# Optimization experiments

Hardware: AMD Instinct MI355X
Metric: run time of the kernel (lower is better)

## Reference

```python
import jax, jax.numpy as jnp
import numpy as np

D_EMBED = 1024
D_CROSS = 768
N_HEADS = 16
D_HEAD = D_EMBED // N_HEADS


def setup_inputs() -> dict:
    key = jax.random.key(0)
    ks = jax.random.split(key, 10)
    s = 0.02
    return {
        "x": jax.random.normal(ks[0], (4, 4096, D_EMBED), dtype=jnp.float32),
        "y": jax.random.normal(ks[1], (4, 1024, D_CROSS), dtype=jnp.float32),
        "Wq": jax.random.normal(ks[2], (D_EMBED, D_EMBED), dtype=jnp.float32) * s,
        "bq": jnp.zeros((D_EMBED,), dtype=jnp.float32),
        "Wk": jax.random.normal(ks[3], (D_CROSS, D_EMBED), dtype=jnp.float32) * s,
        "bk": jnp.zeros((D_EMBED,), dtype=jnp.float32),
        "Wv": jax.random.normal(ks[4], (D_CROSS, D_EMBED), dtype=jnp.float32) * s,
        "bv": jnp.zeros((D_EMBED,), dtype=jnp.float32),
        "Wo": jax.random.normal(ks[5], (D_EMBED, D_EMBED), dtype=jnp.float32) * s,
        "bo": jnp.zeros((D_EMBED,), dtype=jnp.float32),
    }


def reference(x, y, Wq, bq, Wk, bk, Wv, bv, Wo, bo):
    b, sq, _ = x.shape
    skv = y.shape[1]
    # projections
    q = x @ Wq + bq   # [b, sq, d_embed]
    k = y @ Wk + bk   # [b, skv, d_embed]
    v = y @ Wv + bv   # [b, skv, d_embed]
    # split heads: [b, h, s, d_head]
    q = q.reshape(b, sq, N_HEADS, D_HEAD).transpose(0, 2, 1, 3)
    k = k.reshape(b, skv, N_HEADS, D_HEAD).transpose(0, 2, 1, 3)
    v = v.reshape(b, skv, N_HEADS, D_HEAD).transpose(0, 2, 1, 3)
    scale = 1.0 / jnp.sqrt(jnp.float32(D_HEAD))
    scores = jnp.einsum("bhqd,bhkd->bhqk", q, k) * scale
    attn = jax.nn.softmax(scores, axis=-1)
    out = jnp.einsum("bhqk,bhkd->bhqd", attn, v)
    out = out.transpose(0, 2, 1, 3).reshape(b, sq, D_EMBED)
    return out @ Wo + bo
```

## Files before the change

kernel.cpp:

```cpp
#include <hip/hip_runtime.h>

typedef unsigned short ushort_t;
typedef __attribute__((ext_vector_type(8))) __bf16 bf16x8;
typedef __attribute__((ext_vector_type(4))) float floatx4;
typedef __attribute__((ext_vector_type(8))) unsigned short ushortx8;
typedef __attribute__((ext_vector_type(4))) unsigned short ushortx4;
typedef __attribute__((ext_vector_type(4))) short short4v;
typedef __attribute__((ext_vector_type(2))) unsigned uint2v;

__device__ __forceinline__ ushort_t f2bf(float f) {
    union { float f; unsigned u; } v; v.f = f;
    unsigned r = v.u + 0x7fffu + ((v.u >> 16) & 1u);
    return (ushort_t)(r >> 16);
}

__device__ __forceinline__ void gld_lds16(const ushort_t* g, ushort_t* l) {
    __builtin_amdgcn_global_load_lds(
        (const __attribute__((address_space(1))) unsigned*)g,
        (__attribute__((address_space(3))) unsigned*)l, 16, 0, 0);
}

__device__ __forceinline__ unsigned pk_bf16(float a, float b) {
    unsigned ua = __builtin_bit_cast(unsigned, a) + 0x8000u;
    unsigned ub = __builtin_bit_cast(unsigned, b) + 0x8000u;
    return __builtin_amdgcn_perm(ub, ua, 0x07060302u);
}

__global__ __launch_bounds__(256) void prep(
    const float* __restrict__ x, const float* __restrict__ y,
    const float* __restrict__ Wq, const float* __restrict__ Wo,
    const float* __restrict__ Wk, const float* __restrict__ Wv,
    ushort_t* __restrict__ xb, ushort_t* __restrict__ yb,
    ushort_t* __restrict__ Wqt, ushort_t* __restrict__ Wot,
    ushort_t* __restrict__ Wkvt) {
    const int bid = blockIdx.x;
    if (bid < 19456) {
        const int NX = 4194304;
        int i = bid * 256 + threadIdx.x;
        float4 v; ushortx4* dst;
        if (i < NX) { v = ((const float4*)x)[i]; dst = (ushortx4*)xb + i; }
        else        { int j = i - NX; v = ((const float4*)y)[j]; dst = (ushortx4*)yb + j; }
        ushortx4 o;
        o.x = f2bf(v.x); o.y = f2bf(v.y); o.z = f2bf(v.z); o.w = f2bf(v.w);
        *dst = o;
        return;
    }
    __shared__ ushort_t t[32][33];
    const float* W; ushort_t* Wt; int K, n0, k0;
    if (bid < 21504) {
        int tt = bid - 19456;
        W = (tt >> 10) ? Wo : Wq;
        Wt = (tt >> 10) ? Wot : Wqt;
        K = 1024;
        int r = tt & 1023;
        n0 = (r & 31) * 32; k0 = (r >> 5) * 32;
    } else {
        int tt = bid - 21504;
        int z = tt / 768, r = tt - z * 768;
        W = z ? Wv : Wk;
        Wt = Wkvt + (size_t)z * 786432;
        K = 768;
        n0 = (r & 31) * 32; k0 = (r >> 5) * 32;
    }
    const int tx = threadIdx.x & 31, ty = threadIdx.x >> 5;
#pragma unroll
    for (int i = 0; i < 4; ++i)
        t[ty + 8 * i][tx] = f2bf(W[(size_t)(k0 + ty + 8 * i) * 1024 + n0 + tx]);
    __syncthreads();
#pragma unroll
    for (int i = 0; i < 4; ++i)
        Wt[(size_t)(n0 + ty + 8 * i) * K + k0 + tx] = t[tx][ty + 8 * i];
}

__device__ __forceinline__ void gemm_core(
    const ushort_t* __restrict__ A, const ushort_t* __restrict__ Bt,
    int K, int m0, int n0, ushort_t* As, ushort_t* Bs,
    floatx4 (&acc)[4][4], int tid, int wr, int wc, int quad, int l16) {
    const ushort_t* ga0 = A + (size_t)(m0 + (tid >> 2)) * K + (tid & 3) * 8;
    const ushort_t* ga1 = A + (size_t)(m0 + 64 + (tid >> 2)) * K + (tid & 3) * 8;
    const ushort_t* gb0 = Bt + (size_t)(n0 + (tid >> 2)) * K + (tid & 3) * 8;
    const ushort_t* gb1 = Bt + (size_t)(n0 + 64 + (tid >> 2)) * K + (tid & 3) * 8;
    ushort_t* la0 = As + tid * 8;
    ushort_t* la1 = As + (tid + 256) * 8;
    ushort_t* lb0 = Bs + tid * 8;
    ushort_t* lb1 = Bs + (tid + 256) * 8;

    for (int kt = 0; kt < K; kt += 32) {
        __syncthreads();
        gld_lds16(ga0, la0); gld_lds16(ga1, la1);
        gld_lds16(gb0, lb0); gld_lds16(gb1, lb1);
        ga0 += 32; ga1 += 32; gb0 += 32; gb1 += 32;
        __syncthreads();
        bf16x8 af[4], bfr[4];
#pragma unroll
        for (int i = 0; i < 4; ++i)
            af[i] = *(const bf16x8*)(As + (wr * 64 + i * 16 + l16) * 32 + quad * 8);
#pragma unroll
        for (int j = 0; j < 4; ++j)
            bfr[j] = *(const bf16x8*)(Bs + (wc * 64 + j * 16 + l16) * 32 + quad * 8);
#pragma unroll
        for (int i = 0; i < 4; ++i)
#pragma unroll
            for (int j = 0; j < 4; ++j)
                acc[i][j] = __builtin_amdgcn_mfma_f32_16x16x32_bf16(af[i], bfr[j], acc[i][j], 0, 0, 0);
    }
}

__global__ __launch_bounds__(256) void proj(
    const ushort_t* __restrict__ xb, const ushort_t* __restrict__ yb,
    const ushort_t* __restrict__ Wqt, const ushort_t* __restrict__ Wkvt,
    const float* __restrict__ bq, const float* __restrict__ bk, const float* __restrict__ bv,
    ushort_t* __restrict__ Qc, ushort_t* __restrict__ Kc, ushort_t* __restrict__ Vc,
    float qscale) {
    __shared__ __align__(16) ushort_t As[128 * 32];
    __shared__ __align__(16) ushort_t Bs[128 * 32];
    const int tid = threadIdx.x;
    const int lane = tid & 63, w = tid >> 6;
    const int quad = lane >> 4, l16 = lane & 15;
    const int wr = w >> 1, wc = w & 1;
    const int id = blockIdx.x;
    floatx4 acc[4][4] = {};

    if (id < 1024) {
        const int m0 = (id >> 3) * 128, n0 = (id & 7) * 128;
        gemm_core(xb, Wqt, 1024, m0, n0, As, Bs, acc, tid, wr, wc, quad, l16);
#pragma unroll
        for (int i = 0; i < 4; ++i) {
            const int rowb = m0 + wr * 64 + i * 16 + quad * 4;
#pragma unroll
            for (int j = 0; j < 4; ++j) {
                const int col = n0 + wc * 64 + j * 16 + l16;
                const float bval = bq[col];
                const int h = col >> 6, d = col & 63;
                const int b_ = rowb >> 12, q = rowb & 4095;
                ushort_t* base = Qc +
                    (((size_t)b_ * 16 + h) * 32 + (q >> 7)) * 8192 +
                    (d >> 3) * 1024 + (size_t)(q & 127) * 8 + (d & 7);
#pragma unroll
                for (int r = 0; r < 4; ++r)
                    base[r * 8] = f2bf((acc[i][j][r] + bval) * qscale);
            }
        }
    } else {
        const int id2 = id - 1024;
        const int m0 = (id2 & 31) * 128, n0 = (id2 >> 5) * 128;
        gemm_core(yb, Wkvt, 768, m0, n0, As, Bs, acc, tid, wr, wc, quad, l16);
        if (n0 < 1024) {
#pragma unroll
            for (int i = 0; i < 4; ++i) {
                const int rowb = m0 + wr * 64 + i * 16 + quad * 4;
                const int b = rowb >> 10, kvt = (rowb & 1023) >> 6, kvr = rowb & 63;
#pragma unroll
                for (int j = 0; j < 4; ++j) {
                    const int col = n0 + wc * 64 + j * 16 + l16;
                    const int h = col >> 6, d = col & 63;
                    const float bval = bk[col];
                    ushort_t* base = Kc + (((size_t)b * 16 + h) * 16 + kvt) * 4096 +
                                     (d >> 3) * 512 + kvr * 8 + (d & 7);
#pragma unroll
                    for (int r = 0; r < 4; ++r)
                        base[r * 8] = f2bf(acc[i][j][r] + bval);
                }
            }
        } else {
#pragma unroll
            for (int i = 0; i < 4; ++i) {
                const int rowb = m0 + wr * 64 + i * 16 + quad * 4;
                const int b = rowb >> 10, kvt = (rowb & 1023) >> 6, sub = (rowb >> 3) & 7;
#pragma unroll
                for (int j = 0; j < 4; ++j) {
                    const int col = n0 + wc * 64 + j * 16 + l16;
                    const int nc = col - 1024;
                    const int h = nc >> 6, d = nc & 63;
                    const float bval = bv[nc];
                    ushortx4 o;
#pragma unroll
                    for (int r = 0; r < 4; ++r) o[r] = f2bf(acc[i][j][r] + bval);
                    *(ushortx4*)(Vc + (((size_t)b * 16 + h) * 16 + kvt) * 4096 +
                                 sub * 512 + d * 8 + (quad & 1) * 4) = o;
                }
            }
        }
    }
}

__global__ __launch_bounds__(256) void gemm_o(
    const ushort_t* __restrict__ A, const ushort_t* __restrict__ Bt,
    const float* __restrict__ bias, float* __restrict__ C, int N, int K) {
    __shared__ __align__(16) ushort_t As[128 * 32];
    __shared__ __align__(16) ushort_t Bs[128 * 32];
    const int tid = threadIdx.x;
    const int lane = tid & 63, w = tid >> 6;
    const int quad = lane >> 4, l16 = lane & 15;
    const int wr = w >> 1, wc = w & 1;
    const int m0 = blockIdx.x * 128, n0 = blockIdx.y * 128;
    floatx4 acc[4][4] = {};
    gemm_core(A, Bt, K, m0, n0, As, Bs, acc, tid, wr, wc, quad, l16);
#pragma unroll
    for (int i = 0; i < 4; ++i) {
        const int rowb = m0 + wr * 64 + i * 16 + quad * 4;
#pragma unroll
        for (int j = 0; j < 4; ++j) {
            const int col = n0 + wc * 64 + j * 16 + l16;
            const float bval = bias[col];
#pragma unroll
            for (int r = 0; r < 4; ++r)
                C[(size_t)(rowb + r) * N + col] = acc[i][j][r] + bval;
        }
    }
}

__device__ __forceinline__ void stage_kv(const ushort_t* kg, const ushort_t* vg,
                                         ushort_t* dst, int tid) {
#pragma unroll
    for (int i = 0; i < 2; ++i) {
        int s = i * 256 + tid;
        gld_lds16(kg + s * 8, dst + s * 8);
        gld_lds16(vg + s * 8, dst + 4096 + s * 8);
    }
}

__global__ __launch_bounds__(256, 4) void attn_kernel(
    const ushort_t* __restrict__ Qc,
    const ushort_t* __restrict__ Kc,
    const ushort_t* __restrict__ Vc,
    ushort_t* __restrict__ O)
{
    __shared__ __align__(16) ushort_t smem[16384];
    const int tid = threadIdx.x;
    const int w = tid >> 6, lane = tid & 63;
    const int quad = lane >> 4, l16 = lane & 15;
    const int q0 = blockIdx.x * 128;
    const int bh = blockIdx.y, b = bh >> 4;

    const ushort_t* qg = Qc + ((size_t)bh * 32 + blockIdx.x) * 8192;
    bf16x8 qf[2][2];
#pragma unroll
    for (int ks = 0; ks < 2; ++ks)
#pragma unroll
        for (int qt = 0; qt < 2; ++qt)
            qf[ks][qt] = *(const bf16x8*)(qg +
                ((ks * 4 + quad) * 128 + w * 32 + qt * 16 + l16) * 8);

    const ushort_t* kvbase = Kc + (size_t)bh * 65536;
    const ushort_t* vvbase = Vc + (size_t)bh * 65536;
    stage_kv(kvbase, vvbase, smem, tid);
    __syncthreads();

    floatx4 oacc[4][2] = {};
    float lsum[2] = {0.f, 0.f};

    for (int kvt = 0; kvt < 16; ++kvt) {
        const int sel = kvt & 1;
        if (kvt < 15)
            stage_kv(kvbase + (kvt + 1) * 4096, vvbase + (kvt + 1) * 4096,
                     smem + (sel ^ 1) * 8192, tid);
        const ushort_t* pK = smem + sel * 8192;
        const ushort_t* pV = pK + 4096;

        floatx4 st[4][2] = {};
#pragma unroll
        for (int ks = 0; ks < 2; ++ks) {
            bf16x8 ak[4];
#pragma unroll
            for (int m4 = 0; m4 < 4; ++m4)
                ak[m4] = *(const bf16x8*)(pK + ((ks * 4 + quad) * 64 + m4 * 16 + l16) * 8);
#pragma unroll
            for (int m4 = 0; m4 < 4; ++m4)
#pragma unroll
                for (int qt = 0; qt < 2; ++qt)
                    st[m4][qt] = __builtin_amdgcn_mfma_f32_16x16x32_bf16(ak[m4], qf[ks][qt], st[m4][qt], 0, 0, 0);
        }

        uint2v pk[4][2];
#pragma unroll
        for (int qt = 0; qt < 2; ++qt) {
            float acc = 0.f;
#pragma unroll
            for (int m4 = 0; m4 < 4; ++m4) {
                float p0 = __builtin_amdgcn_exp2f(st[m4][qt][0]);
                float p1 = __builtin_amdgcn_exp2f(st[m4][qt][1]);
                float p2 = __builtin_amdgcn_exp2f(st[m4][qt][2]);
                float p3 = __builtin_amdgcn_exp2f(st[m4][qt][3]);
                acc += (p0 + p1) + (p2 + p3);
                pk[m4][qt].x = pk_bf16(p0, p1);
                pk[m4][qt].y = pk_bf16(p2, p3);
            }
            lsum[qt] += acc;
        }

#pragma unroll
        for (int m4 = 0; m4 < 4; ++m4) {
#pragma unroll
            for (int dt = 0; dt < 4; ++dt) {
                short4v av = *(const short4v*)(pV +
                    ((m4 * 2 + (quad >> 1)) * 64 + dt * 16 + l16) * 8 + (quad & 1) * 4);
#pragma unroll
                for (int qt = 0; qt < 2; ++qt) {
                    short4v bp = __builtin_bit_cast(short4v, pk[m4][qt]);
                    oacc[dt][qt] = __builtin_amdgcn_mfma_f32_16x16x16bf16_1k(av, bp, oacc[dt][qt], 0, 0, 0);
                }
            }
        }
        __syncthreads();
    }

    const int h = bh & 15;
    float inv[2];
#pragma unroll
    for (int qt = 0; qt < 2; ++qt) {
        float l = lsum[qt];
        l += __shfl_xor(l, 16, 64);
        l += __shfl_xor(l, 32, 64);
        inv[qt] = 1.0f / l;
    }
#pragma unroll
    for (int dt = 0; dt < 4; ++dt)
#pragma unroll
        for (int qt = 0; qt < 2; ++qt) {
            uint2v o2;
            o2.x = pk_bf16(oacc[dt][qt][0] * inv[qt], oacc[dt][qt][1] * inv[qt]);
            o2.y = pk_bf16(oacc[dt][qt][2] * inv[qt], oacc[dt][qt][3] * inv[qt]);
            *(uint2v*)(smem + (w * 32 + qt * 16 + l16) * 68 + dt * 16 + quad * 4) = o2;
        }
    __syncthreads();
#pragma unroll
    for (int i = 0; i < 8; ++i) {
        int s = i * 256 + tid;
        int row = s >> 4, dc = s & 15;
        ushortx4 v = *(const ushortx4*)(smem + row * 68 + dc * 4);
        *(ushortx4*)(O + (size_t)(b * 4096 + q0 + row) * 1024 + h * 64 + dc * 4) = v;
    }
}

extern "C" void kernel_launch(void* const* d_in, const int* in_sizes, int n_in,
                              void* d_out, int out_size, void* d_ws, size_t ws_size,
                              hipStream_t stream) {
    const float* x  = (const float*)d_in[0];
    const float* y  = (const float*)d_in[1];
    const float* Wq = (const float*)d_in[2];
    const float* bq = (const float*)d_in[3];
    const float* Wk = (const float*)d_in[4];
    const float* bk = (const float*)d_in[5];
    const float* Wv = (const float*)d_in[6];
    const float* bv = (const float*)d_in[7];
    const float* Wo = (const float*)d_in[8];
    const float* bo = (const float*)d_in[9];

    char* ws = (char*)d_ws;
    ushort_t* xb   = (ushort_t*)(ws);
    ushort_t* yb   = (ushort_t*)(ws + 33554432);
    ushort_t* Wqt  = (ushort_t*)(ws + 39845888);
    ushort_t* Wkvt = (ushort_t*)(ws + 41943040);
    ushort_t* Wot  = (ushort_t*)(ws + 45088768);
    ushort_t* Qc   = (ushort_t*)(ws + 47185920);
    ushort_t* Kc   = (ushort_t*)(ws + 80740352);
    ushort_t* Vc   = (ushort_t*)(ws + 89128960);
    ushort_t* Ab   = (ushort_t*)(ws + 97517568);

    const float QSCALE = 0.125f * 1.44269504f;

    prep<<<23040, 256, 0, stream>>>(x, y, Wq, Wo, Wk, Wv, xb, yb, Wqt, Wot, Wkvt);
    proj<<<1536, 256, 0, stream>>>(xb, yb, Wqt, Wkvt, bq, bk, bv, Qc, Kc, Vc, QSCALE);
    attn_kernel<<<dim3(32, 64), 256, 0, stream>>>(Qc, Kc, Vc, Ab);
    gemm_o<<<dim3(128, 8), 256, 0, stream>>>(Ab, Wot, bo, (float*)d_out, 1024, 1024);
}
```

Before: 365.7 us.

## Fuse all four stages into one persistent kernel with grid barriers

Replaces the prep, projection, attention and output-GEMM launches with a single persistent kernel of 1024 blocks. The stages are separated by atomic-counter grid barriers, and the projection tiles are handed out dynamically through an atomic work counter. The bf16 copy of x now shares a buffer with the attention output, and the GEMM LDS reads get an XOR swizzle to reduce bank conflicts. This removes launch gaps and tail effects between stages. In exchange it adds barrier spin costs, relies on all 1024 blocks being co-resident (launch bounds 256,4), and fixes the occupancy for every stage.

```diff
diff --git a/kernel.cpp b/kernel.cpp
--- a/kernel.cpp
+++ b/kernel.cpp
@@ -3,7 +3,6 @@
 typedef unsigned short ushort_t;
 typedef __attribute__((ext_vector_type(8))) __bf16 bf16x8;
 typedef __attribute__((ext_vector_type(4))) float floatx4;
-typedef __attribute__((ext_vector_type(8))) unsigned short ushortx8;
 typedef __attribute__((ext_vector_type(4))) unsigned short ushortx4;
 typedef __attribute__((ext_vector_type(4))) short short4v;
 typedef __attribute__((ext_vector_type(2))) unsigned uint2v;
@@ -26,60 +25,27 @@
     return __builtin_amdgcn_perm(ub, ua, 0x07060302u);
 }
 
-__global__ __launch_bounds__(256) void prep(
-    const float* __restrict__ x, const float* __restrict__ y,
-    const float* __restrict__ Wq, const float* __restrict__ Wo,
-    const float* __restrict__ Wk, const float* __restrict__ Wv,
-    ushort_t* __restrict__ xb, ushort_t* __restrict__ yb,
-    ushort_t* __restrict__ Wqt, ushort_t* __restrict__ Wot,
-    ushort_t* __restrict__ Wkvt) {
-    const int bid = blockIdx.x;
-    if (bid < 19456) {
-        const int NX = 4194304;
-        int i = bid * 256 + threadIdx.x;
-        float4 v; ushortx4* dst;
-        if (i < NX) { v = ((const float4*)x)[i]; dst = (ushortx4*)xb + i; }
-        else        { int j = i - NX; v = ((const float4*)y)[j]; dst = (ushortx4*)yb + j; }
-        ushortx4 o;
-        o.x = f2bf(v.x); o.y = f2bf(v.y); o.z = f2bf(v.z); o.w = f2bf(v.w);
-        *dst = o;
-        return;
-    }
-    __shared__ ushort_t t[32][33];
-    const float* W; ushort_t* Wt; int K, n0, k0;
-    if (bid < 21504) {
-        int tt = bid - 19456;
-        W = (tt >> 10) ? Wo : Wq;
-        Wt = (tt >> 10) ? Wot : Wqt;
-        K = 1024;
-        int r = tt & 1023;
-        n0 = (r & 31) * 32; k0 = (r >> 5) * 32;
-    } else {
-        int tt = bid - 21504;
-        int z = tt / 768, r = tt - z * 768;
-        W = z ? Wv : Wk;
-        Wt = Wkvt + (size_t)z * 786432;
-        K = 768;
-        n0 = (r & 31) * 32; k0 = (r >> 5) * 32;
-    }
-    const int tx = threadIdx.x & 31, ty = threadIdx.x >> 5;
-#pragma unroll
-    for (int i = 0; i < 4; ++i)
-        t[ty + 8 * i][tx] = f2bf(W[(size_t)(k0 + ty + 8 * i) * 1024 + n0 + tx]);
-    __syncthreads();
-#pragma unroll
-    for (int i = 0; i < 4; ++i)
-        Wt[(size_t)(n0 + ty + 8 * i) * K + k0 + tx] = t[tx][ty + 8 * i];
-}
-
-__device__ __forceinline__ void gemm_core(
+__device__ __forceinline__ void gridbar(unsigned* ctr, int tid) {
+    __syncthreads();
+    if (tid == 0) {
+        __hip_atomic_fetch_add(ctr, 1u, __ATOMIC_ACQ_REL, __HIP_MEMORY_SCOPE_AGENT);
+        while (__hip_atomic_load(ctr, __ATOMIC_ACQUIRE, __HIP_MEMORY_SCOPE_AGENT) < 1024u)
+            __builtin_amdgcn_s_sleep(2);
+    }
+    __syncthreads();
+}
+
+__device__ __forceinline__ void gemm_core128(
     const ushort_t* __restrict__ A, const ushort_t* __restrict__ Bt,
     int K, int m0, int n0, ushort_t* As, ushort_t* Bs,
     floatx4 (&acc)[4][4], int tid, int wr, int wc, int quad, int l16) {
-    const ushort_t* ga0 = A + (size_t)(m0 + (tid >> 2)) * K + (tid & 3) * 8;
-    const ushort_t* ga1 = A + (size_t)(m0 + 64 + (tid >> 2)) * K + (tid & 3) * 8;
-    const ushort_t* gb0 = Bt + (size_t)(n0 + (tid >> 2)) * K + (tid & 3) * 8;
-    const ushort_t* gb1 = Bt + (size_t)(n0 + 64 + (tid >> 2)) * K + (tid & 3) * 8;
+    const int cx = (quad ^ ((l16 >> 1) & 3)) * 8;
+    const int ra = tid >> 2;
+    const int ka = (tid & 3) ^ ((tid >> 3) & 3);
+    const ushort_t* ga0 = A + (size_t)(m0 + ra) * K + ka * 8;
+    const ushort_t* ga1 = A + (size_t)(m0 + 64 + ra) * K + ka * 8;
+    const ushort_t* gb0 = Bt + (size_t)(n0 + ra) * K + ka * 8;
+    const ushort_t* gb1 = Bt + (size_t)(n0 + 64 + ra) * K + ka * 8;
     ushort_t* la0 = As + tid * 8;
     ushort_t* la1 = As + (tid + 256) * 8;
     ushort_t* lb0 = Bs + tid * 8;
@@ -94,10 +60,10 @@
         bf16x8 af[4], bfr[4];
 #pragma unroll
         for (int i = 0; i < 4; ++i)
-            af[i] = *(const bf16x8*)(As + (wr * 64 + i * 16 + l16) * 32 + quad * 8);
+            af[i] = *(const bf16x8*)(As + (wr * 64 + i * 16 + l16) * 32 + cx);
 #pragma unroll
         for (int j = 0; j < 4; ++j)
-            bfr[j] = *(const bf16x8*)(Bs + (wc * 64 + j * 16 + l16) * 32 + quad * 8);
+            bfr[j] = *(const bf16x8*)(Bs + (wc * 64 + j * 16 + l16) * 32 + cx);
 #pragma unroll
         for (int i = 0; i < 4; ++i)
 #pragma unroll
@@ -106,134 +72,18 @@
     }
 }
 
-__global__ __launch_bounds__(256) void proj(
-    const ushort_t* __restrict__ xb, const ushort_t* __restrict__ yb,
-    const ushort_t* __restrict__ Wqt, const ushort_t* __restrict__ Wkvt,
-    const float* __restrict__ bq, const float* __restrict__ bk, const float* __restrict__ bv,
-    ushort_t* __restrict__ Qc, ushort_t* __restrict__ Kc, ushort_t* __restrict__ Vc,
-    float qscale) {
-    __shared__ __align__(16) ushort_t As[128 * 32];
-    __shared__ __align__(16) ushort_t Bs[128 * 32];
-    const int tid = threadIdx.x;
-    const int lane = tid & 63, w = tid >> 6;
-    const int quad = lane >> 4, l16 = lane & 15;
-    const int wr = w >> 1, wc = w & 1;
-    const int id = blockIdx.x;
-    floatx4 acc[4][4] = {};
-
-    if (id < 1024) {
-        const int m0 = (id >> 3) * 128, n0 = (id & 7) * 128;
-        gemm_core(xb, Wqt, 1024, m0, n0, As, Bs, acc, tid, wr, wc, quad, l16);
-#pragma unroll
-        for (int i = 0; i < 4; ++i) {
-            const int rowb = m0 + wr * 64 + i * 16 + quad * 4;
-#pragma unroll
-            for (int j = 0; j < 4; ++j) {
-                const int col = n0 + wc * 64 + j * 16 + l16;
-                const float bval = bq[col];
-                const int h = col >> 6, d = col & 63;
-                const int b_ = rowb >> 12, q = rowb & 4095;
-                ushort_t* base = Qc +
-                    (((size_t)b_ * 16 + h) * 32 + (q >> 7)) * 8192 +
-                    (d >> 3) * 1024 + (size_t)(q & 127) * 8 + (d & 7);
-#pragma unroll
-                for (int r = 0; r < 4; ++r)
-                    base[r * 8] = f2bf((acc[i][j][r] + bval) * qscale);
-            }
-        }
-    } else {
-        const int id2 = id - 1024;
-        const int m0 = (id2 & 31) * 128, n0 = (id2 >> 5) * 128;
-        gemm_core(yb, Wkvt, 768, m0, n0, As, Bs, acc, tid, wr, wc, quad, l16);
-        if (n0 < 1024) {
-#pragma unroll
-            for (int i = 0; i < 4; ++i) {
-                const int rowb = m0 + wr * 64 + i * 16 + quad * 4;
-                const int b = rowb >> 10, kvt = (rowb & 1023) >> 6, kvr = rowb & 63;
-#pragma unroll
-                for (int j = 0; j < 4; ++j) {
-                    const int col = n0 + wc * 64 + j * 16 + l16;
-                    const int h = col >> 6, d = col & 63;
-                    const float bval = bk[col];
-                    ushort_t* base = Kc + (((size_t)b * 16 + h) * 16 + kvt) * 4096 +
-                                     (d >> 3) * 512 + kvr * 8 + (d & 7);
-#pragma unroll
-                    for (int r = 0; r < 4; ++r)
-                        base[r * 8] = f2bf(acc[i][j][r] + bval);
-                }
-            }
-        } else {
-#pragma unroll
-            for (int i = 0; i < 4; ++i) {
-                const int rowb = m0 + wr * 64 + i * 16 + quad * 4;
-                const int b = rowb >> 10, kvt = (rowb & 1023) >> 6, sub = (rowb >> 3) & 7;
-#pragma unroll
-                for (int j = 0; j < 4; ++j) {
-                    const int col = n0 + wc * 64 + j * 16 + l16;
-                    const int nc = col - 1024;
-                    const int h = nc >> 6, d = nc & 63;
-                    const float bval = bv[nc];
-                    ushortx4 o;
-#pragma unroll
-                    for (int r = 0; r < 4; ++r) o[r] = f2bf(acc[i][j][r] + bval);
-                    *(ushortx4*)(Vc + (((size_t)b * 16 + h) * 16 + kvt) * 4096 +
-                                 sub * 512 + d * 8 + (quad & 1) * 4) = o;
-                }
-            }
-        }
-    }
-}
-
-__global__ __launch_bounds__(256) void gemm_o(
-    const ushort_t* __restrict__ A, const ushort_t* __restrict__ Bt,
-    const float* __restrict__ bias, float* __restrict__ C, int N, int K) {
-    __shared__ __align__(16) ushort_t As[128 * 32];
-    __shared__ __align__(16) ushort_t Bs[128 * 32];
-    const int tid = threadIdx.x;
-    const int lane = tid & 63, w = tid >> 6;
-    const int quad = lane >> 4, l16 = lane & 15;
-    const int wr = w >> 1, wc = w & 1;
-    const int m0 = blockIdx.x * 128, n0 = blockIdx.y * 128;
-    floatx4 acc[4][4] = {};
-    gemm_core(A, Bt, K, m0, n0, As, Bs, acc, tid, wr, wc, quad, l16);
-#pragma unroll
-    for (int i = 0; i < 4; ++i) {
-        const int rowb = m0 + wr * 64 + i * 16 + quad * 4;
-#pragma unroll
-        for (int j = 0; j < 4; ++j) {
-            const int col = n0 + wc * 64 + j * 16 + l16;
-            const float bval = bias[col];
-#pragma unroll
-            for (int r = 0; r < 4; ++r)
-                C[(size_t)(rowb + r) * N + col] = acc[i][j][r] + bval;
-        }
-    }
-}
-
-__device__ __forceinline__ void stage_kv(const ushort_t* kg, const ushort_t* vg,
-                                         ushort_t* dst, int tid) {
-#pragma unroll
-    for (int i = 0; i < 2; ++i) {
-        int s = i * 256 + tid;
-        gld_lds16(kg + s * 8, dst + s * 8);
-        gld_lds16(vg + s * 8, dst + 4096 + s * 8);
-    }
-}
-
-__global__ __launch_bounds__(256, 4) void attn_kernel(
-    const ushort_t* __restrict__ Qc,
-    const ushort_t* __restrict__ Kc,
-    const ushort_t* __restrict__ Vc,
-    ushort_t* __restrict__ O)
-{
-    __shared__ __align__(16) ushort_t smem[16384];
-    const int tid = threadIdx.x;
+__device__ __forceinline__ void attn_phase(
+    const ushort_t* __restrict__ Qc, const ushort_t* __restrict__ Kc,
+    const ushort_t* __restrict__ Vc, ushort_t* __restrict__ O,
+    int q0blk, int bh, int tid, ushort_t* smem) {
     const int w = tid >> 6, lane = tid & 63;
     const int quad = lane >> 4, l16 = lane & 15;
-    const int q0 = blockIdx.x * 128;
-    const int bh = blockIdx.y, b = bh >> 4;
-
-    const ushort_t* qg = Qc + ((size_t)bh * 32 + blockIdx.x) * 8192;
+    const int q0 = q0blk * 128;
+    const int b = bh >> 4;
+
+    __syncthreads();
+
+    const ushort_t* qg = Qc + ((size_t)bh * 32 + q0blk) * 8192;
     bf16x8 qf[2][2];
 #pragma unroll
     for (int ks = 0; ks < 2; ++ks)
@@ -244,7 +94,12 @@
 
     const ushort_t* kvbase = Kc + (size_t)bh * 65536;
     const ushort_t* vvbase = Vc + (size_t)bh * 65536;
-    stage_kv(kvbase, vvbase, smem, tid);
+#pragma unroll
+    for (int i = 0; i < 2; ++i) {
+        int s = i * 256 + tid;
+        gld_lds16(kvbase + s * 8, smem + s * 8);
+        gld_lds16(vvbase + s * 8, smem + 4096 + s * 8);
+    }
     __syncthreads();
 
     floatx4 oacc[4][2] = {};
@@ -252,9 +107,17 @@
 
     for (int kvt = 0; kvt < 16; ++kvt) {
         const int sel = kvt & 1;
-        if (kvt < 15)
-            stage_kv(kvbase + (kvt + 1) * 4096, vvbase + (kvt + 1) * 4096,
-                     smem + (sel ^ 1) * 8192, tid);
+        if (kvt < 15) {
+            const ushort_t* kg = kvbase + (kvt + 1) * 4096;
+            const ushort_t* vg = vvbase + (kvt + 1) * 4096;
+            ushort_t* dst = smem + (sel ^ 1) * 8192;
+#pragma unroll
+            for (int i = 0; i < 2; ++i) {
+                int s = i * 256 + tid;
+                gld_lds16(kg + s * 8, dst + s * 8);
+                gld_lds16(vg + s * 8, dst + 4096 + s * 8);
+            }
+        }
         const ushort_t* pK = smem + sel * 8192;
         const ushort_t* pV = pK + 4096;
 
@@ -330,6 +193,169 @@
         int row = s >> 4, dc = s & 15;
         ushortx4 v = *(const ushortx4*)(smem + row * 68 + dc * 4);
         *(ushortx4*)(O + (size_t)(b * 4096 + q0 + row) * 1024 + h * 64 + dc * 4) = v;
+    }
+}
+
+__global__ __launch_bounds__(256, 4) void fused(
+    const float* __restrict__ x, const float* __restrict__ y,
+    const float* __restrict__ Wq, const float* __restrict__ bq,
+    const float* __restrict__ Wk, const float* __restrict__ bk,
+    const float* __restrict__ Wv, const float* __restrict__ bv,
+    const float* __restrict__ Wo, const float* __restrict__ bo,
+    ushort_t* __restrict__ yb, ushort_t* __restrict__ Wqt,
+    ushort_t* __restrict__ Wkvt, ushort_t* __restrict__ Wot,
+    ushort_t* __restrict__ Qc, ushort_t* __restrict__ Kc,
+    ushort_t* __restrict__ Vc, ushort_t* __restrict__ AbX,
+    unsigned* __restrict__ cnt, float* __restrict__ out) {
+    __shared__ __align__(16) ushort_t smem[16384];
+    __shared__ unsigned vslot;
+    const int tid = threadIdx.x, bid = blockIdx.x;
+    const float QSCALE = 0.125f * 1.44269504f;
+
+    {
+#pragma unroll 1
+        for (int s = 0; s < 19; ++s) {
+            int i = s * 262144 + bid * 256 + tid;
+            float4 v; ushortx4* dst;
+            if (i < 4194304) { v = ((const float4*)x)[i]; dst = (ushortx4*)AbX + i; }
+            else             { int j = i - 4194304; v = ((const float4*)y)[j]; dst = (ushortx4*)yb + j; }
+            ushortx4 o;
+            o.x = f2bf(v.x); o.y = f2bf(v.y); o.z = f2bf(v.z); o.w = f2bf(v.w);
+            *dst = o;
+        }
+        ushort_t (*t)[33] = (ushort_t(*)[33])smem;
+        const int tx = tid & 31, ty = tid >> 5;
+#pragma unroll 1
+        for (int s = 0; s < 4; ++s) {
+            int wv = s * 1024 + bid;
+            if (wv < 3584) {
+                const float* W; ushort_t* Wt; int K, n0, k0;
+                if (wv < 2048) {
+                    W = (wv >> 10) ? Wo : Wq; Wt = (wv >> 10) ? Wot : Wqt; K = 1024;
+                    int r = wv & 1023; n0 = (r & 31) * 32; k0 = (r >> 5) * 32;
+                } else {
+                    int t2 = wv - 2048; int z = t2 / 768, r = t2 - z * 768;
+                    W = z ? Wv : Wk; Wt = Wkvt + (size_t)z * 786432; K = 768;
+                    n0 = (r & 31) * 32; k0 = (r >> 5) * 32;
+                }
+                __syncthreads();
+#pragma unroll
+                for (int i = 0; i < 4; ++i)
+                    t[ty + 8 * i][tx] = f2bf(W[(size_t)(k0 + ty + 8 * i) * 1024 + n0 + tx]);
+                __syncthreads();
+#pragma unroll
+                for (int i = 0; i < 4; ++i)
+                    Wt[(size_t)(n0 + ty + 8 * i) * K + k0 + tx] = t[tx][ty + 8 * i];
+            }
+        }
+    }
+    gridbar(cnt + 1, tid);
+
+    {
+        const int lane = tid & 63, w = tid >> 6;
+        const int quad = lane >> 4, l16 = lane & 15;
+        const int wr = w >> 1, wc = w & 1;
+        ushort_t* As = smem;
+        ushort_t* Bs = smem + 4096;
+        for (;;) {
+            __syncthreads();
+            if (tid == 0)
+                vslot = __hip_atomic_fetch_add(cnt, 1u, __ATOMIC_RELAXED, __HIP_MEMORY_SCOPE_AGENT);
+            __syncthreads();
+            const unsigned v = vslot;
+            if (v >= 1536u) break;
+            floatx4 acc[4][4] = {};
+            if (v < 1024u) {
+                const int m0 = (int)(v >> 3) * 128, n0 = (int)(v & 7) * 128;
+                gemm_core128(AbX, Wqt, 1024, m0, n0, As, Bs, acc, tid, wr, wc, quad, l16);
+#pragma unroll
+                for (int i = 0; i < 4; ++i) {
+                    const int rowb = m0 + wr * 64 + i * 16 + quad * 4;
+                    const int b_ = rowb >> 12, q = rowb & 4095;
+#pragma unroll
+                    for (int j = 0; j < 4; ++j) {
+                        const int col = n0 + wc * 64 + j * 16 + l16;
+                        const float bval = bq[col];
+                        const int h = col >> 6, d = col & 63;
+                        ushort_t* base = Qc +
+                            (((size_t)b_ * 16 + h) * 32 + (q >> 7)) * 8192 +
+                            (d >> 3) * 1024 + (size_t)(q & 127) * 8 + (d & 7);
+#pragma unroll
+                        for (int r = 0; r < 4; ++r)
+                            base[r * 8] = f2bf((acc[i][j][r] + bval) * QSCALE);
+                    }
+                }
+            } else {
+                const int kv = (int)v - 1024;
+                const int m0 = (kv >> 4) * 128, n0 = (kv & 15) * 128;
+                gemm_core128(yb, Wkvt, 768, m0, n0, As, Bs, acc, tid, wr, wc, quad, l16);
+                if (n0 < 1024) {
+#pragma unroll
+                    for (int i = 0; i < 4; ++i) {
+                        const int rowb = m0 + wr * 64 + i * 16 + quad * 4;
+                        const int b = rowb >> 10, kvt = (rowb & 1023) >> 6, kvr = rowb & 63;
+#pragma unroll
+                        for (int j = 0; j < 4; ++j) {
+                            const int col = n0 + wc * 64 + j * 16 + l16;
+                            const int h = col >> 6, d = col & 63;
+                            const float bval = bk[col];
+                            ushort_t* base = Kc + (((size_t)b * 16 + h) * 16 + kvt) * 4096 +
+                                             (d >> 3) * 512 + kvr * 8 + (d & 7);
+#pragma unroll
+                            for (int r = 0; r < 4; ++r)
+                                base[r * 8] = f2bf(acc[i][j][r] + bval);
+                        }
+                    }
+                } else {
+#pragma unroll
+                    for (int i = 0; i < 4; ++i) {
+                        const int rowb = m0 + wr * 64 + i * 16 + quad * 4;
+                        const int b = rowb >> 10, kvt = (rowb & 1023) >> 6, sub = (rowb >> 3) & 7;
+#pragma unroll
+                        for (int j = 0; j < 4; ++j) {
+                            const int col = n0 + wc * 64 + j * 16 + l16;
+                            const int nc = col - 1024;
+                            const int h = nc >> 6, d = nc & 63;
+                            const float bval = bv[nc];
+                            ushortx4 o;
+#pragma unroll
+                            for (int r = 0; r < 4; ++r) o[r] = f2bf(acc[i][j][r] + bval);
+                            *(ushortx4*)(Vc + (((size_t)b * 16 + h) * 16 + kvt) * 4096 +
+                                         sub * 512 + d * 8 + (quad & 1) * 4) = o;
+                        }
+                    }
+                }
+            }
+        }
+    }
+    gridbar(cnt + 2, tid);
+
+#pragma unroll 1
+    for (int s = 0; s < 2; ++s) {
+        const int a = s * 1024 + bid;
+        attn_phase(Qc, Kc, Vc, AbX, a & 31, a >> 5, tid, smem);
+    }
+    gridbar(cnt + 3, tid);
+
+    {
+        const int lane = tid & 63, w = tid >> 6;
+        const int quad = lane >> 4, l16 = lane & 15;
+        const int wr = w >> 1, wc = w & 1;
+        const int m0 = (bid >> 3) * 128, n0 = (bid & 7) * 128;
+        floatx4 acc[4][4] = {};
+        gemm_core128(AbX, Wot, 1024, m0, n0, smem, smem + 4096, acc, tid, wr, wc, quad, l16);
+#pragma unroll
+        for (int i = 0; i < 4; ++i) {
+            const int rowb = m0 + wr * 64 + i * 16 + quad * 4;
+#pragma unroll
+            for (int j = 0; j < 4; ++j) {
+                const int col = n0 + wc * 64 + j * 16 + l16;
+                const float bval = bo[col];
+#pragma unroll
+                for (int r = 0; r < 4; ++r)
+                    out[(size_t)(rowb + r) * 1024 + col] = acc[i][j][r] + bval;
+            }
+        }
     }
 }
 
@@ -348,20 +374,18 @@
     const float* bo = (const float*)d_in[9];
 
     char* ws = (char*)d_ws;
-    ushort_t* xb   = (ushort_t*)(ws);
-    ushort_t* yb   = (ushort_t*)(ws + 33554432);
-    ushort_t* Wqt  = (ushort_t*)(ws + 39845888);
-    ushort_t* Wkvt = (ushort_t*)(ws + 41943040);
-    ushort_t* Wot  = (ushort_t*)(ws + 45088768);
-    ushort_t* Qc   = (ushort_t*)(ws + 47185920);
-    ushort_t* Kc   = (ushort_t*)(ws + 80740352);
-    ushort_t* Vc   = (ushort_t*)(ws + 89128960);
-    ushort_t* Ab   = (ushort_t*)(ws + 97517568);
-
-    const float QSCALE = 0.125f * 1.44269504f;
-
-    prep<<<23040, 256, 0, stream>>>(x, y, Wq, Wo, Wk, Wv, xb, yb, Wqt, Wot, Wkvt);
-    proj<<<1536, 256, 0, stream>>>(xb, yb, Wqt, Wkvt, bq, bk, bv, Qc, Kc, Vc, QSCALE);
-    attn_kernel<<<dim3(32, 64), 256, 0, stream>>>(Qc, Kc, Vc, Ab);
-    gemm_o<<<dim3(128, 8), 256, 0, stream>>>(Ab, Wot, bo, (float*)d_out, 1024, 1024);
-}
+    unsigned* cnt  = (unsigned*)(ws);
+    ushort_t* yb   = (ushort_t*)(ws + 64);
+    ushort_t* Wqt  = (ushort_t*)(ws + 6291520);
+    ushort_t* Wkvt = (ushort_t*)(ws + 8388672);
+    ushort_t* Wot  = (ushort_t*)(ws + 11534400);
+    ushort_t* Qc   = (ushort_t*)(ws + 13631552);
+    ushort_t* Kc   = (ushort_t*)(ws + 47185984);
+    ushort_t* Vc   = (ushort_t*)(ws + 55574592);
+    ushort_t* AbX  = (ushort_t*)(ws + 63963200);
+
+    hipMemsetAsync(cnt, 0, 64, stream);
+    fused<<<1024, 256, 0, stream>>>(x, y, Wq, bq, Wk, bk, Wv, bv, Wo, bo,
+                                    yb, Wqt, Wkvt, Wot, Qc, Kc, Vc, AbX,
+                                    cnt, (float*)d_out);
+}
```

New measurement: 1.109 ms. 3.03x slower.
